# Performance work log

Hardware: AMD Instinct MI355X
Metric: run time of the kernel (lower is better)

The kernel has to match this reference:

```python
import jax, jax.numpy as jnp
import numpy as np

D_MODEL = 1024
HEADS = 16
DEPTH = D_MODEL // HEADS
B, S = 4, 4096
EPS_K = 1e-6  # kernel feature epsilon
EPS_LN = 1e-6


def setup_inputs() -> dict:
    key = jax.random.key(0)
    ks = jax.random.split(key, 8)
    lecun = 1.0 / np.sqrt(D_MODEL)  # LecunNormal stddev
    glorot = np.sqrt(2.0 / (D_MODEL + D_MODEL))  # keras Dense default
    return {
        "q": jax.random.normal(ks[0], (B, S, D_MODEL), jnp.float32),
        "k": jax.random.normal(ks[1], (B, S, D_MODEL), jnp.float32),
        "v": jax.random.normal(ks[2], (B, S, D_MODEL), jnp.float32),
        "mask": jnp.ones((B, S), jnp.float32),
        "wq": jax.random.normal(ks[3], (D_MODEL, D_MODEL), jnp.float32) * lecun,
        "wk": jax.random.normal(ks[4], (D_MODEL, D_MODEL), jnp.float32) * lecun,
        "wv": jax.random.normal(ks[5], (D_MODEL, D_MODEL), jnp.float32) * lecun,
        "ln_gamma": jnp.ones((D_MODEL,), jnp.float32),
        "ln_beta": jnp.zeros((D_MODEL,), jnp.float32),
        "dense_w": jax.random.normal(ks[6], (D_MODEL, D_MODEL), jnp.float32) * glorot,
        "dense_b": jnp.zeros((D_MODEL,), jnp.float32),
    }


def _layernorm(x, g, b):
    m = jnp.mean(x, axis=-1, keepdims=True)
    var = jnp.var(x, axis=-1, keepdims=True)
    return (x - m) * jax.lax.rsqrt(var + EPS_LN) * g + b


def _split_heads(x):
    bsz, sl, _ = x.shape
    return x.reshape(bsz, sl, HEADS, DEPTH).transpose(0, 2, 1, 3)  # [B,H,S,depth]


def reference(q, k, v, mask, wq, wk, wv, ln_gamma, ln_beta, dense_w, dense_b):
    bsz = q.shape[0]
    em = mask[:, None, :, None]  # [B,1,S,1] broadcast over heads/depth
    qh = _split_heads(_layernorm(q @ wq, ln_gamma, ln_beta))
    kh = _split_heads(_layernorm(k @ wk, ln_gamma, ln_beta))
    vh = _split_heads(_layernorm(v @ wv, ln_gamma, ln_beta))
    q_prime = jax.nn.relu(qh) + EPS_K
    k_prime = (jax.nn.relu(kh) + EPS_K) * em
    vh = vh * em
    kv = jnp.einsum('bhnd,bhne->bhde', k_prime, vh)  # [B,H,depth,depth]
    z = 1.0 / (jnp.einsum('bhnd,bhd->bhn', q_prime, k_prime.sum(axis=-2)) + EPS_K)
    att = jnp.einsum('bhnd,bhde,bhn->bhne', q_prime, kv, z)  # [B,H,S,depth]
    # Faithful to original: reshape WITHOUT transposing heads back.
    att = att.reshape(bsz, -1, D_MODEL)  # [B,S,d_model]
    out = att @ dense_w + dense_b
    return _layernorm(out, ln_gamma, ln_beta)
```

## Files before the change

kernel.cpp:

```cpp
#include <hip/hip_runtime.h>
#include <hip/hip_bf16.h>
#include <stdint.h>

#define D_MODEL 1024
#define S_LEN   4096
#define BATCH   4
#define HEADS   16
#define DEPTH   64
#define ROWS    (BATCH*S_LEN)
#define EPS_K_F 1e-6f
#define EPS_LN_F 1e-6f

typedef __attribute__((ext_vector_type(8))) short short8;
typedef __attribute__((ext_vector_type(4))) float f32x4;

__device__ __forceinline__ unsigned short f2bf(float f) {
  union { float f; unsigned u; } x; x.f = f;
  unsigned r = x.u + 0x7FFF + ((x.u >> 16) & 1);
  return (unsigned short)(r >> 16);
}
__device__ __forceinline__ float bf2f(unsigned short b) {
  union { unsigned u; float f; } x; x.u = ((unsigned)b) << 16;
  return x.f;
}
__device__ __forceinline__ void gload16(const void* g, void* l) {
  __builtin_amdgcn_global_load_lds(
      (const __attribute__((address_space(1))) void*)g,
      (__attribute__((address_space(3))) void*)l, 16, 0, 0);
}

__global__ __launch_bounds__(256) void cvt_f32_bf16_k(
    const float* __restrict__ in, unsigned short* __restrict__ out, int n4) {
  int i = blockIdx.x * 256 + threadIdx.x;
  if (i < n4) {
    float4 v = ((const float4*)in)[i];
    ushort4 o;
    o.x = f2bf(v.x); o.y = f2bf(v.y); o.z = f2bf(v.z); o.w = f2bf(v.w);
    ((ushort4*)out)[i] = o;
  }
}

__global__ __launch_bounds__(256) void wtrans_k(
    const float* __restrict__ W, unsigned short* __restrict__ Wt) {
  __shared__ float tile[32][33];
  int n0 = blockIdx.x * 32, k0 = blockIdx.y * 32;
  int tx = threadIdx.x & 31, ty = threadIdx.x >> 5;
  #pragma unroll
  for (int i = 0; i < 32; i += 8)
    tile[ty + i][tx] = W[(size_t)(k0 + ty + i) * D_MODEL + n0 + tx];
  __syncthreads();
  #pragma unroll
  for (int i = 0; i < 32; i += 8)
    Wt[(size_t)(n0 + ty + i) * D_MODEL + k0 + tx] = f2bf(tile[tx][ty + i]);
}


#define GEMM_EPILOGUE(HASBIAS)                                               \
  if (HASBIAS) {                                                             \
    float bv[4];                                                             \
    _Pragma("unroll")                                                        \
    for (int n = 0; n < 4; ++n)                                              \
      bv[n] = bias[(int)n0 + wcn * 64 + n * 16 + l15];                       \
    _Pragma("unroll")                                                        \
    for (int m = 0; m < 8; ++m)                                              \
      _Pragma("unroll")                                                      \
      for (int n = 0; n < 4; ++n)                                            \
        _Pragma("unroll")                                                    \
        for (int j = 0; j < 4; ++j)                                          \
          acc[m][n][j] += bv[n];                                             \
  }                                                                          \
  int seg = (int)(n0 >> 6) + wcn;                                            \
  _Pragma("unroll")                                                          \
  for (int m = 0; m < 8; ++m) {                                              \
    float s[4], s2[4];                                                       \
    _Pragma("unroll")                                                        \
    for (int j = 0; j < 4; ++j) {                                            \
      float a = 0.f, b = 0.f;                                                \
      _Pragma("unroll")                                                      \
      for (int n = 0; n < 4; ++n) { float x = acc[m][n][j]; a += x; b += x*x; } \
      s[j] = a; s2[j] = b;                                                   \
    }                                                                        \
    _Pragma("unroll")                                                        \
    for (int off = 1; off < 16; off <<= 1) {                                 \
      _Pragma("unroll")                                                      \
      for (int j = 0; j < 4; ++j) {                                          \
        s[j]  += __shfl_xor(s[j],  off);                                     \
        s2[j] += __shfl_xor(s2[j], off);                                     \
      }                                                                      \
    }                                                                        \
    if (l15 == 0) {                                                          \
      _Pragma("unroll")                                                      \
      for (int j = 0; j < 4; ++j) {                                          \
        int rg = (int)m0 + wr * 128 + m * 16 + lhi * 4 + j;                  \
        psum[rg * 16 + seg] = s[j];                                          \
        psq [rg * 16 + seg] = s2[j];                                         \
      }                                                                      \
    }                                                                        \
  }                                                                          \
  _Pragma("unroll")                                                          \
  for (int m = 0; m < 8; ++m)                                                \
    _Pragma("unroll")                                                        \
    for (int j = 0; j < 4; ++j) {                                            \
      size_t row = m0 + wr * 128 + m * 16 + lhi * 4 + j;                     \
      _Pragma("unroll")                                                      \
      for (int n = 0; n < 4; ++n) {                                          \
        int col = (int)n0 + wcn * 64 + n * 16 + l15;                         \
        Cb[row * N + col] = f2bf(acc[m][n][j]);                              \
      }                                                                      \
    }

#define STAGE_HALF(kof_, slot_, h_) do {                                     \
    _Pragma("unroll")                                                        \
    for (int j = 0; j < 2; ++j) {                                            \
      int idx = j * 512 + t; int r_ = idx >> 2; int cs_ = idx & 3;           \
      int c_ = cs_ ^ ((r_ >> 1) & 3);                                        \
      gload16(A + (m0 + r_) * (size_t)K + (kof_) + (h_) * 32 + c_ * 8,       \
              &Al[slot_][(h_) * 8192 + idx * 8]);                            \
    }                                                                        \
    _Pragma("unroll")                                                        \
    for (int j = 0; j < 2; ++j) {                                            \
      int idx = j * 512 + t; int r_ = idx >> 2; int cs_ = idx & 3;           \
      int c_ = cs_ ^ ((r_ >> 1) & 3);                                        \
      gload16(Bt + (n0 + r_) * (size_t)K + (kof_) + (h_) * 32 + c_ * 8,      \
              &Bl[slot_][(h_) * 8192 + idx * 8]);                            \
    }                                                                        \
  } while (0)

#define PH_READ_B(kk_)                                                       \
    _Pragma("unroll")                                                        \
    for (int n = 0; n < 4; ++n) {                                            \
      int rb_ = wcn * 64 + n * 16 + l15;                                     \
      bfr[n] = *(const short8*)&Bl[slot][(kk_) * 8192 + rb_ * 32 + cswz];    \
    }
#define PH_READ_A(kk_, mh_)                                                  \
    _Pragma("unroll")                                                        \
    for (int m = 0; m < 4; ++m) {                                            \
      int ra_ = wr * 128 + ((mh_) * 4 + m) * 16 + l15;                       \
      af[m] = *(const short8*)&Al[slot][(kk_) * 8192 + ra_ * 32 + cswz];     \
    }
#define PH_MFMA(mh_)                                                         \
    __builtin_amdgcn_s_setprio(1);                                           \
    _Pragma("unroll")                                                        \
    for (int m = 0; m < 4; ++m)                                              \
      _Pragma("unroll")                                                      \
      for (int n = 0; n < 4; ++n)                                            \
        acc[(mh_) * 4 + m][n] = __builtin_amdgcn_mfma_f32_16x16x32_bf16(     \
            af[m], bfr[n], acc[(mh_) * 4 + m][n], 0, 0, 0);                  \
    __builtin_amdgcn_s_setprio(0);
#define LGKM0                                                                \
    asm volatile("s_waitcnt lgkmcnt(0)" ::: "memory");                       \
    __builtin_amdgcn_sched_barrier(0);

#define SIDE_PACK_STORE(chunk_) do {                                         \
    uint4 pk_;                                                               \
    pk_.x = (unsigned)f2bf(sreg0.x) | ((unsigned)f2bf(sreg0.y) << 16);       \
    pk_.y = (unsigned)f2bf(sreg0.z) | ((unsigned)f2bf(sreg0.w) << 16);       \
    pk_.z = (unsigned)f2bf(sreg1.x) | ((unsigned)f2bf(sreg1.y) << 16);       \
    pk_.w = (unsigned)f2bf(sreg1.z) | ((unsigned)f2bf(sreg1.w) << 16);       \
    *(uint4*)(side_dst + sbase + (size_t)(chunk_) * 4096) = pk_;             \
  } while (0)
#define SIDE_LOAD(chunk_) do {                                               \
    const float* sp_ = side_src + sbase + (size_t)(chunk_) * 4096;           \
    sreg0 = *(const float4*)sp_; sreg1 = *(const float4*)(sp_ + 4);          \
  } while (0)

#define TAIL_TILE(slot_) do {                                                \
    const int slot = (slot_);                                                \
    short8 af[4], bfr[4];                                                    \
    PH_READ_B(0) PH_READ_A(0, 0) LGKM0 PH_MFMA(0)                            \
    PH_READ_A(0, 1) LGKM0 PH_MFMA(1)                                         \
    PH_READ_B(1) PH_READ_A(1, 0) LGKM0 PH_MFMA(0)                            \
    PH_READ_A(1, 1) LGKM0 PH_MFMA(1)                                         \
  } while (0)

template <bool SIDECAR>
__global__ __launch_bounds__(512) void gemm_bt_k(
    const unsigned short* __restrict__ A,
    const unsigned short* __restrict__ Bt,
    unsigned short* __restrict__ Cb,
    float* __restrict__ psum, float* __restrict__ psq,
    const float* __restrict__ bias,
    const float* __restrict__ side_src,
    unsigned short* __restrict__ side_dst,
    int M, int N, int K) {
  __shared__ unsigned short Al[2][16384];
  __shared__ unsigned short Bl[2][16384];
  int t = threadIdx.x;
  int lane = t & 63, wid = t >> 6;
  int wr = wid >> 2, wcn = wid & 3;
  int l15 = lane & 15, lhi = lane >> 4;
  const int cswz = (lhi ^ ((l15 >> 1) & 3)) << 3;
  int p = blockIdx.x;
  int cb = (p >> 3) & 3;
  int rb = (p & 7) | ((p >> 5) << 3);
  size_t m0 = (size_t)rb * 256, n0 = (size_t)cb * 256;
  f32x4 acc[8][4] = {};

  const int KT = K >> 6;

  float4 sreg0 = {}, sreg1 = {};
  size_t sbase = (size_t)p * 65536 + (size_t)t * 8;

  if (SIDECAR) SIDE_LOAD(0);
  STAGE_HALF(0, 0, 0);  STAGE_HALF(0, 0, 1);
  STAGE_HALF(64, 1, 0); STAGE_HALF(64, 1, 1);
  asm volatile("s_waitcnt vmcnt(8)" ::: "memory");
  __builtin_amdgcn_s_barrier();
  __builtin_amdgcn_sched_barrier(0);

  for (int kt = 0; kt < KT - 2; ++kt) {
    const int slot = kt & 1;
    short8 af[4], bfr[4];
    PH_READ_B(0)
    PH_READ_A(0, 0)
    LGKM0
    PH_MFMA(0)
    PH_READ_A(0, 1)
    LGKM0
    __builtin_amdgcn_s_barrier();
    __builtin_amdgcn_sched_barrier(0);
    STAGE_HALF((kt + 2) << 6, slot, 0);
    __builtin_amdgcn_sched_barrier(0);
    PH_MFMA(1)
    PH_READ_B(1)
    PH_READ_A(1, 0)
    LGKM0
    PH_MFMA(0)
    PH_READ_A(1, 1)
    LGKM0
    __builtin_amdgcn_s_barrier();
    __builtin_amdgcn_sched_barrier(0);
    STAGE_HALF((kt + 2) << 6, slot, 1);
    __builtin_amdgcn_sched_barrier(0);
    PH_MFMA(1)
    if (SIDECAR) {
      SIDE_PACK_STORE(kt);
      SIDE_LOAD(kt + 1);
      __builtin_amdgcn_sched_barrier(0);
      asm volatile("s_waitcnt vmcnt(11)" ::: "memory");
    } else {
      asm volatile("s_waitcnt vmcnt(8)" ::: "memory");
    }
    __builtin_amdgcn_s_barrier();
    __builtin_amdgcn_sched_barrier(0);
  }

  TAIL_TILE((KT - 2) & 1);
  if (SIDECAR) {
    SIDE_PACK_STORE(KT - 2);
    SIDE_LOAD(KT - 1);
    __builtin_amdgcn_sched_barrier(0);
    asm volatile("s_waitcnt vmcnt(3)" ::: "memory");
  } else {
    asm volatile("s_waitcnt vmcnt(0)" ::: "memory");
  }
  __builtin_amdgcn_s_barrier();
  __builtin_amdgcn_sched_barrier(0);

  TAIL_TILE((KT - 1) & 1);
  if (SIDECAR) SIDE_PACK_STORE(KT - 1);

  GEMM_EPILOGUE(bias != nullptr)
}

__global__ __launch_bounds__(256) void ln_act_k(
    const unsigned short* __restrict__ Cb,
    const float* __restrict__ psum, const float* __restrict__ psq,
    const float* __restrict__ gamma, const float* __restrict__ beta,
    const float* __restrict__ mask,
    unsigned short* __restrict__ out, int mode) {
  int row = blockIdx.x;
  int t = threadIdx.x;
  float s = 0.f, s2 = 0.f;
  #pragma unroll
  for (int i = 0; i < 16; ++i) { s += psum[row * 16 + i]; s2 += psq[row * 16 + i]; }
  float mean = s * (1.f / D_MODEL);
  float var = s2 * (1.f / D_MODEL) - mean * mean;
  float rstd = rsqrtf(var + EPS_LN_F);
  float mk = (mode > 0) ? mask[row] : 1.f;
  ushort4 cv = ((const ushort4*)(Cb + (size_t)row * D_MODEL))[t];
  float4 gv = ((const float4*)gamma)[t];
  float4 bv = ((const float4*)beta)[t];
  float av[4] = {bf2f(cv.x), bf2f(cv.y), bf2f(cv.z), bf2f(cv.w)};
  float g4[4] = {gv.x, gv.y, gv.z, gv.w};
  float b4[4] = {bv.x, bv.y, bv.z, bv.w};
  unsigned short ov[4];
  #pragma unroll
  for (int j = 0; j < 4; ++j) {
    float ln = (av[j] - mean) * rstd * g4[j] + b4[j];
    if (mode == 0)      ln = fmaxf(ln, 0.f) + EPS_K_F;
    else if (mode == 1) ln = (fmaxf(ln, 0.f) + EPS_K_F) * mk;
    else                ln = ln * mk;
    ov[j] = f2bf(ln);
  }
  ushort4 o; o.x = ov[0]; o.y = ov[1]; o.z = ov[2]; o.w = ov[3];
  ((ushort4*)(out + (size_t)row * D_MODEL))[t] = o;
}

__global__ __launch_bounds__(256) void ln_final_k(
    const unsigned short* __restrict__ Cb,
    const float* __restrict__ psum, const float* __restrict__ psq,
    const float* __restrict__ gamma, const float* __restrict__ beta,
    float* __restrict__ out) {
  int row = blockIdx.x;
  int t = threadIdx.x;
  float s = 0.f, s2 = 0.f;
  #pragma unroll
  for (int i = 0; i < 16; ++i) { s += psum[row * 16 + i]; s2 += psq[row * 16 + i]; }
  float mean = s * (1.f / D_MODEL);
  float var = s2 * (1.f / D_MODEL) - mean * mean;
  float rstd = rsqrtf(var + EPS_LN_F);
  ushort4 cv = ((const ushort4*)(Cb + (size_t)row * D_MODEL))[t];
  float4 gv = ((const float4*)gamma)[t];
  float4 bv = ((const float4*)beta)[t];
  float4 w;
  w.x = (bf2f(cv.x) - mean) * rstd * gv.x + bv.x;
  w.y = (bf2f(cv.y) - mean) * rstd * gv.y + bv.y;
  w.z = (bf2f(cv.z) - mean) * rstd * gv.z + bv.z;
  w.w = (bf2f(cv.w) - mean) * rstd * gv.w + bv.w;
  ((float4*)(out + (size_t)row * D_MODEL))[t] = w;
}

__global__ __launch_bounds__(256) void kv_mfma_k(
    const unsigned short* __restrict__ Kp, const unsigned short* __restrict__ Vp,
    float* __restrict__ part, float* __restrict__ kspart) {
  __shared__ unsigned short Kl[4096];
  __shared__ unsigned short Vl[4096];
  int bh = blockIdx.y, chunk = blockIdx.x;
  int b_ = bh >> 4, h = bh & 15;
  int t = threadIdx.x, lane = t & 63, w = t >> 6;
  int l15 = lane & 15, g = lane >> 4;

  int sn = t >> 2, sd16 = t & 3;
  int sc = sd16 ^ ((sn >> 3) & 3);
  size_t goff = (size_t)sn * D_MODEL + h * DEPTH + sd16 * 16;
  int ldst = sn * 64 + sc * 16;

  short8 ones;
  #pragma unroll
  for (int i = 0; i < 8; ++i) ones[i] = (short)0x3F80;

  f32x4 acc[4] = {};
  f32x4 ks = {};

  int baseA = ((w ^ g) << 4) + l15;
  int baseB0 = ((0 ^ g) << 4) + l15;
  int baseB1 = ((1 ^ g) << 4) + l15;
  int baseB2 = ((2 ^ g) << 4) + l15;
  int baseB3 = ((3 ^ g) << 4) + l15;

  size_t rowbase = ((size_t)b_ * S_LEN + (size_t)chunk * 512) * D_MODEL;
  for (int tile = 0; tile < 8; ++tile) {
    const unsigned short* kg = Kp + rowbase + (size_t)tile * 64 * D_MODEL + goff;
    const unsigned short* vg = Vp + rowbase + (size_t)tile * 64 * D_MODEL + goff;
    uint4 ra = *(const uint4*)kg;
    uint4 rb = *(const uint4*)(kg + 8);
    uint4 rc = *(const uint4*)vg;
    uint4 rd = *(const uint4*)(vg + 8);
    __syncthreads();
    *(uint4*)&Kl[ldst]     = ra;
    *(uint4*)&Kl[ldst + 8] = rb;
    *(uint4*)&Vl[ldst]     = rc;
    *(uint4*)&Vl[ldst + 8] = rd;
    __syncthreads();
    #pragma unroll
    for (int kk = 0; kk < 2; ++kk) {
      int nb = (kk * 32 + g * 8) * 64;
      short8 af, bf0, bf1, bf2, bf3;
      #pragma unroll
      for (int i = 0; i < 8; ++i) {
        int rowoff = nb + i * 64;
        af[i]  = (short)Kl[rowoff + baseA];
        bf0[i] = (short)Vl[rowoff + baseB0];
        bf1[i] = (short)Vl[rowoff + baseB1];
        bf2[i] = (short)Vl[rowoff + baseB2];
        bf3[i] = (short)Vl[rowoff + baseB3];
      }
      acc[0] = __builtin_amdgcn_mfma_f32_16x16x32_bf16(af, bf0, acc[0], 0, 0, 0);
      acc[1] = __builtin_amdgcn_mfma_f32_16x16x32_bf16(af, bf1, acc[1], 0, 0, 0);
      acc[2] = __builtin_amdgcn_mfma_f32_16x16x32_bf16(af, bf2, acc[2], 0, 0, 0);
      acc[3] = __builtin_amdgcn_mfma_f32_16x16x32_bf16(af, bf3, acc[3], 0, 0, 0);
      ks     = __builtin_amdgcn_mfma_f32_16x16x32_bf16(af, ones, ks, 0, 0, 0);
    }
  }
  float* pp = part + ((size_t)bh * 8 + chunk) * 4096;
  #pragma unroll
  for (int nf = 0; nf < 4; ++nf)
    #pragma unroll
    for (int r = 0; r < 4; ++r)
      pp[(16 * w + 4 * g + r) * 64 + 16 * nf + l15] = acc[nf][r];
  if (l15 == 0) {
    #pragma unroll
    for (int r = 0; r < 4; ++r)
      kspart[((size_t)bh * 8 + chunk) * 64 + 16 * w + 4 * g + r] = ks[r];
  }
}

__global__ __launch_bounds__(256) void kv_reduce_k(
    const float* __restrict__ part, const float* __restrict__ kspart,
    unsigned short* __restrict__ KVT, float* __restrict__ ksum) {
  int bh = blockIdx.x, t = threadIdx.x;
  for (int idx = t; idx < 4096; idx += 256) {
    int d = idx >> 6, e = idx & 63;
    float s = 0.f;
    #pragma unroll
    for (int c = 0; c < 8; ++c)
      s += part[((size_t)bh * 8 + c) * 4096 + d * 64 + e];
    KVT[(size_t)bh * 4096 + e * 64 + d] = f2bf(s);
  }
  if (t < 64) {
    float s = 0.f;
    #pragma unroll
    for (int c = 0; c < 8; ++c) s += kspart[((size_t)bh * 8 + c) * 64 + t];
    ksum[bh * 64 + t] = s;
  }
}

__global__ __launch_bounds__(256) void att_k(
    const unsigned short* __restrict__ Qp, const unsigned short* __restrict__ KVT,
    const float* __restrict__ ksum, unsigned short* __restrict__ att) {
  __shared__ unsigned short Ql[128 * 64];
  __shared__ unsigned short Kl[64 * 64];
  __shared__ float ksl[64];
  __shared__ float zl[128];
  int bh = blockIdx.y;
  int b = bh >> 4, h = bh & 15;
  int r0 = blockIdx.x * 128;
  int t = threadIdx.x, lane = t & 63, wid = t >> 6;
  int l15 = lane & 15, lhi = lane >> 4;
  #pragma unroll
  for (int i = 0; i < 4; ++i) {
    int cid = i * 256 + t;
    int r = cid >> 3, c8 = cid & 7;
    gload16(Qp + ((size_t)(b * S_LEN + r0 + r)) * D_MODEL + h * DEPTH + c8 * 8,
            &Ql[cid * 8]);
  }
  #pragma unroll
  for (int i = 0; i < 2; ++i) {
    int cid = i * 256 + t;
    gload16(KVT + (size_t)bh * 4096 + cid * 8, &Kl[cid * 8]);
  }
  if (t < 64) ksl[t] = ksum[bh * 64 + t];
  asm volatile("s_waitcnt vmcnt(0)" ::: "memory");
  __syncthreads();
  {
    int r = t >> 1, half = t & 1;
    float s = 0.f;
    #pragma unroll
    for (int j = 0; j < 32; ++j)
      s += bf2f(Ql[r * 64 + half * 32 + j]) * ksl[half * 32 + j];
    s += __shfl_xor(s, 1);
    if (half == 0) zl[r] = 1.f / (s + EPS_K_F);
  }
  __syncthreads();
  f32x4 acc[2][4] = {};
  #pragma unroll
  for (int kk = 0; kk < 2; ++kk) {
    short8 af[2], bfr[4];
    #pragma unroll
    for (int m = 0; m < 2; ++m)
      af[m] = *(const short8*)&Ql[(wid * 32 + m * 16 + l15) * 64 + kk * 32 + lhi * 8];
    #pragma unroll
    for (int n = 0; n < 4; ++n)
      bfr[n] = *(const short8*)&Kl[(n * 16 + l15) * 64 + kk * 32 + lhi * 8];
    #pragma unroll
    for (int m = 0; m < 2; ++m)
      #pragma unroll
      for (int n = 0; n < 4; ++n)
        acc[m][n] = __builtin_amdgcn_mfma_f32_16x16x32_bf16(af[m], bfr[n], acc[m][n], 0, 0, 0);
  }
  #pragma unroll
  for (int m = 0; m < 2; ++m)
    #pragma unroll
    for (int j = 0; j < 4; ++j) {
      int rl = wid * 32 + m * 16 + lhi * 4 + j;
      int n = r0 + rl;
      float z = zl[rl];
      #pragma unroll
      for (int nf = 0; nf < 4; ++nf) {
        int ee = nf * 16 + l15;
        size_t orow = (size_t)b * S_LEN + h * 256 + (n >> 4);
        int ocol = (n & 15) * 64 + ee;
        att[orow * D_MODEL + ocol] = f2bf(acc[m][nf][j] * z);
      }
    }
}

extern "C" void kernel_launch(void* const* d_in, const int* in_sizes, int n_in,
                              void* d_out, int out_size, void* d_ws, size_t ws_size,
                              hipStream_t stream) {
  (void)in_sizes; (void)n_in; (void)out_size; (void)ws_size;
  const float* q     = (const float*)d_in[0];
  const float* k     = (const float*)d_in[1];
  const float* v     = (const float*)d_in[2];
  const float* mask  = (const float*)d_in[3];
  const float* wq    = (const float*)d_in[4];
  const float* wk    = (const float*)d_in[5];
  const float* wv    = (const float*)d_in[6];
  const float* gamma = (const float*)d_in[7];
  const float* beta  = (const float*)d_in[8];
  const float* dw    = (const float*)d_in[9];
  const float* db    = (const float*)d_in[10];
  float* out = (float*)d_out;

  char* ws = (char*)d_ws;
  unsigned short* Xq  = (unsigned short*)(ws);
  unsigned short* Xk  = (unsigned short*)(ws + 33554432);
  unsigned short* Xv  = (unsigned short*)(ws + 67108864);
  unsigned short* Qp  = Xq;
  unsigned short* Kp  = Xk;
  unsigned short* Vp  = Xv;
  unsigned short* Cd  = Xq;
  unsigned short* WqT = (unsigned short*)(ws + 100663296);
  unsigned short* WkT = WqT + 1048576;
  unsigned short* WvT = WkT + 1048576;
  unsigned short* WdT = WvT + 1048576;
  float* part   = (float*)(ws + 109051904);
  float* kspart = (float*)(ws + 117440512);
  unsigned short* KVT = (unsigned short*)(ws + 117964800);
  float* ksum = (float*)(ws + 118489088);
  float* psum = (float*)(ws + 119537664);
  float* psq  = (float*)(ws + 120586240);
  unsigned short* Cqkv = (unsigned short*)d_out;

  dim3 b256(256);
  dim3 b512(512);
  int n4 = ROWS * D_MODEL / 4;
  dim3 cvtg(n4 / 256);
  dim3 wtg(32, 32);
  dim3 gemmg(256);
  dim3 lng(ROWS);

  wtrans_k<<<wtg, b256, 0, stream>>>(wq, WqT);
  wtrans_k<<<wtg, b256, 0, stream>>>(wk, WkT);
  wtrans_k<<<wtg, b256, 0, stream>>>(wv, WvT);
  wtrans_k<<<wtg, b256, 0, stream>>>(dw, WdT);

  cvt_f32_bf16_k<<<cvtg, b256, 0, stream>>>(q, Xq, n4);

  gemm_bt_k<true><<<gemmg, b512, 0, stream>>>(Xq, WqT, Cqkv, psum, psq, nullptr,
                                              k, Xk, ROWS, D_MODEL, D_MODEL);
  ln_act_k<<<lng, b256, 0, stream>>>(Cqkv, psum, psq, gamma, beta, nullptr, Qp, 0);

  gemm_bt_k<true><<<gemmg, b512, 0, stream>>>(Xk, WkT, Cqkv, psum, psq, nullptr,
                                              v, Xv, ROWS, D_MODEL, D_MODEL);
  ln_act_k<<<lng, b256, 0, stream>>>(Cqkv, psum, psq, gamma, beta, mask, Kp, 1);

  gemm_bt_k<false><<<gemmg, b512, 0, stream>>>(Xv, WvT, Cqkv, psum, psq, nullptr,
                                               nullptr, nullptr, ROWS, D_MODEL, D_MODEL);
  ln_act_k<<<lng, b256, 0, stream>>>(Cqkv, psum, psq, gamma, beta, mask, Vp, 2);

  kv_mfma_k<<<dim3(8, 64), b256, 0, stream>>>(Kp, Vp, part, kspart);
  kv_reduce_k<<<dim3(64), b256, 0, stream>>>(part, kspart, KVT, ksum);
  att_k<<<dim3(32, 64), b256, 0, stream>>>(Qp, KVT, ksum, Cqkv);

  gemm_bt_k<false><<<gemmg, b512, 0, stream>>>(Cqkv, WdT, Cd, psum, psq, db,
                                               nullptr, nullptr, ROWS, D_MODEL, D_MODEL);
  ln_final_k<<<lng, b256, 0, stream>>>(Cd, psum, psq, gamma, beta, out);
}
```

Measured before the change: 347.3 us.

## Fuse layernorm epilogues into GEMMs using a cooperative grid-wide sync

Each projection GEMM and the final dense GEMM now keep their accumulators in registers. They write per-row partial sums, wait on a cooperative-groups grid barrier, then apply layernorm, activation and mask directly before storing. This removes the intermediate bf16 GEMM output and the four separate layernorm kernels, along with their global memory round-trips and launches. In exchange it needs cooperative launches whose whole grid is resident at once, pays for a grid-wide barrier, and holds the accumulators across that barrier.

New measurement: 488.1 us. 40.5% more time.

```diff
diff --git a/kernel.cpp b/kernel.cpp
--- a/kernel.cpp
+++ b/kernel.cpp
@@ -1,5 +1,6 @@
 #include <hip/hip_runtime.h>
 #include <hip/hip_bf16.h>
+#include <hip/hip_cooperative_groups.h>
 #include <stdint.h>
 
 #define D_MODEL 1024
@@ -11,6 +12,8 @@
 #define EPS_K_F 1e-6f
 #define EPS_LN_F 1e-6f
 
+namespace cg = cooperative_groups;
+
 typedef __attribute__((ext_vector_type(8))) short short8;
 typedef __attribute__((ext_vector_type(4))) float f32x4;
 
@@ -55,73 +58,19 @@
 }
 
 
-#define GEMM_EPILOGUE(HASBIAS)                                               \
-  if (HASBIAS) {                                                             \
-    float bv[4];                                                             \
-    _Pragma("unroll")                                                        \
-    for (int n = 0; n < 4; ++n)                                              \
-      bv[n] = bias[(int)n0 + wcn * 64 + n * 16 + l15];                       \
-    _Pragma("unroll")                                                        \
-    for (int m = 0; m < 8; ++m)                                              \
-      _Pragma("unroll")                                                      \
-      for (int n = 0; n < 4; ++n)                                            \
-        _Pragma("unroll")                                                    \
-        for (int j = 0; j < 4; ++j)                                          \
-          acc[m][n][j] += bv[n];                                             \
-  }                                                                          \
-  int seg = (int)(n0 >> 6) + wcn;                                            \
-  _Pragma("unroll")                                                          \
-  for (int m = 0; m < 8; ++m) {                                              \
-    float s[4], s2[4];                                                       \
-    _Pragma("unroll")                                                        \
-    for (int j = 0; j < 4; ++j) {                                            \
-      float a = 0.f, b = 0.f;                                                \
-      _Pragma("unroll")                                                      \
-      for (int n = 0; n < 4; ++n) { float x = acc[m][n][j]; a += x; b += x*x; } \
-      s[j] = a; s2[j] = b;                                                   \
-    }                                                                        \
-    _Pragma("unroll")                                                        \
-    for (int off = 1; off < 16; off <<= 1) {                                 \
-      _Pragma("unroll")                                                      \
-      for (int j = 0; j < 4; ++j) {                                          \
-        s[j]  += __shfl_xor(s[j],  off);                                     \
-        s2[j] += __shfl_xor(s2[j], off);                                     \
-      }                                                                      \
-    }                                                                        \
-    if (l15 == 0) {                                                          \
-      _Pragma("unroll")                                                      \
-      for (int j = 0; j < 4; ++j) {                                          \
-        int rg = (int)m0 + wr * 128 + m * 16 + lhi * 4 + j;                  \
-        psum[rg * 16 + seg] = s[j];                                          \
-        psq [rg * 16 + seg] = s2[j];                                         \
-      }                                                                      \
-    }                                                                        \
-  }                                                                          \
-  _Pragma("unroll")                                                          \
-  for (int m = 0; m < 8; ++m)                                                \
-    _Pragma("unroll")                                                        \
-    for (int j = 0; j < 4; ++j) {                                            \
-      size_t row = m0 + wr * 128 + m * 16 + lhi * 4 + j;                     \
-      _Pragma("unroll")                                                      \
-      for (int n = 0; n < 4; ++n) {                                          \
-        int col = (int)n0 + wcn * 64 + n * 16 + l15;                         \
-        Cb[row * N + col] = f2bf(acc[m][n][j]);                              \
-      }                                                                      \
-    }
-
 #define STAGE_HALF(kof_, slot_, h_) do {                                     \
     _Pragma("unroll")                                                        \
     for (int j = 0; j < 2; ++j) {                                            \
       int idx = j * 512 + t; int r_ = idx >> 2; int cs_ = idx & 3;           \
       int c_ = cs_ ^ ((r_ >> 1) & 3);                                        \
-      gload16(A + (m0 + r_) * (size_t)K + (kof_) + (h_) * 32 + c_ * 8,       \
+      gload16(A + (m0 + r_) * (size_t)D_MODEL + (kof_) + (h_) * 32 + c_ * 8, \
               &Al[slot_][(h_) * 8192 + idx * 8]);                            \
     }                                                                        \
     _Pragma("unroll")                                                        \
     for (int j = 0; j < 2; ++j) {                                            \
       int idx = j * 512 + t; int r_ = idx >> 2; int cs_ = idx & 3;           \
       int c_ = cs_ ^ ((r_ >> 1) & 3);                                        \
-      gload16(Bt + (n0 + r_) * (size_t)K + (kof_) + (h_) * 32 + c_ * 8,      \
+      gload16(Bt + (n0 + r_) * (size_t)D_MODEL + (kof_) + (h_) * 32 + c_ * 8,\
               &Bl[slot_][(h_) * 8192 + idx * 8]);                            \
     }                                                                        \
   } while (0)
@@ -173,16 +122,17 @@
     PH_READ_A(1, 1) LGKM0 PH_MFMA(1)                                         \
   } while (0)
 
-template <bool SIDECAR>
-__global__ __launch_bounds__(512) void gemm_bt_k(
+template <bool SIDECAR, int MODE>
+__global__ __launch_bounds__(512) void gemm_fused_k(
     const unsigned short* __restrict__ A,
     const unsigned short* __restrict__ Bt,
-    unsigned short* __restrict__ Cb,
     float* __restrict__ psum, float* __restrict__ psq,
     const float* __restrict__ bias,
     const float* __restrict__ side_src,
     unsigned short* __restrict__ side_dst,
-    int M, int N, int K) {
+    const float* __restrict__ gamma, const float* __restrict__ beta,
+    const float* __restrict__ maskp,
+    unsigned short* __restrict__ outb, float* __restrict__ outf) {
   __shared__ unsigned short Al[2][16384];
   __shared__ unsigned short Bl[2][16384];
   int t = threadIdx.x;
@@ -196,7 +146,7 @@
   size_t m0 = (size_t)rb * 256, n0 = (size_t)cb * 256;
   f32x4 acc[8][4] = {};
 
-  const int KT = K >> 6;
+  const int KT = D_MODEL >> 6;
 
   float4 sreg0 = {}, sreg1 = {};
   size_t sbase = (size_t)p * 65536 + (size_t)t * 8;
@@ -260,65 +210,94 @@
   TAIL_TILE((KT - 1) & 1);
   if (SIDECAR) SIDE_PACK_STORE(KT - 1);
 
-  GEMM_EPILOGUE(bias != nullptr)
-}
-
-__global__ __launch_bounds__(256) void ln_act_k(
-    const unsigned short* __restrict__ Cb,
-    const float* __restrict__ psum, const float* __restrict__ psq,
-    const float* __restrict__ gamma, const float* __restrict__ beta,
-    const float* __restrict__ mask,
-    unsigned short* __restrict__ out, int mode) {
-  int row = blockIdx.x;
-  int t = threadIdx.x;
-  float s = 0.f, s2 = 0.f;
-  #pragma unroll
-  for (int i = 0; i < 16; ++i) { s += psum[row * 16 + i]; s2 += psq[row * 16 + i]; }
-  float mean = s * (1.f / D_MODEL);
-  float var = s2 * (1.f / D_MODEL) - mean * mean;
-  float rstd = rsqrtf(var + EPS_LN_F);
-  float mk = (mode > 0) ? mask[row] : 1.f;
-  ushort4 cv = ((const ushort4*)(Cb + (size_t)row * D_MODEL))[t];
-  float4 gv = ((const float4*)gamma)[t];
-  float4 bv = ((const float4*)beta)[t];
-  float av[4] = {bf2f(cv.x), bf2f(cv.y), bf2f(cv.z), bf2f(cv.w)};
-  float g4[4] = {gv.x, gv.y, gv.z, gv.w};
-  float b4[4] = {bv.x, bv.y, bv.z, bv.w};
-  unsigned short ov[4];
-  #pragma unroll
-  for (int j = 0; j < 4; ++j) {
-    float ln = (av[j] - mean) * rstd * g4[j] + b4[j];
-    if (mode == 0)      ln = fmaxf(ln, 0.f) + EPS_K_F;
-    else if (mode == 1) ln = (fmaxf(ln, 0.f) + EPS_K_F) * mk;
-    else                ln = ln * mk;
-    ov[j] = f2bf(ln);
-  }
-  ushort4 o; o.x = ov[0]; o.y = ov[1]; o.z = ov[2]; o.w = ov[3];
-  ((ushort4*)(out + (size_t)row * D_MODEL))[t] = o;
-}
-
-__global__ __launch_bounds__(256) void ln_final_k(
-    const unsigned short* __restrict__ Cb,
-    const float* __restrict__ psum, const float* __restrict__ psq,
-    const float* __restrict__ gamma, const float* __restrict__ beta,
-    float* __restrict__ out) {
-  int row = blockIdx.x;
-  int t = threadIdx.x;
-  float s = 0.f, s2 = 0.f;
-  #pragma unroll
-  for (int i = 0; i < 16; ++i) { s += psum[row * 16 + i]; s2 += psq[row * 16 + i]; }
-  float mean = s * (1.f / D_MODEL);
-  float var = s2 * (1.f / D_MODEL) - mean * mean;
-  float rstd = rsqrtf(var + EPS_LN_F);
-  ushort4 cv = ((const ushort4*)(Cb + (size_t)row * D_MODEL))[t];
-  float4 gv = ((const float4*)gamma)[t];
-  float4 bv = ((const float4*)beta)[t];
-  float4 w;
-  w.x = (bf2f(cv.x) - mean) * rstd * gv.x + bv.x;
-  w.y = (bf2f(cv.y) - mean) * rstd * gv.y + bv.y;
-  w.z = (bf2f(cv.z) - mean) * rstd * gv.z + bv.z;
-  w.w = (bf2f(cv.w) - mean) * rstd * gv.w + bv.w;
-  ((float4*)(out + (size_t)row * D_MODEL))[t] = w;
+  if (MODE == 3) {
+    float bv[4];
+    #pragma unroll
+    for (int n = 0; n < 4; ++n)
+      bv[n] = bias[(int)n0 + wcn * 64 + n * 16 + l15];
+    #pragma unroll
+    for (int m = 0; m < 8; ++m)
+      #pragma unroll
+      for (int n = 0; n < 4; ++n)
+        #pragma unroll
+        for (int j = 0; j < 4; ++j)
+          acc[m][n][j] += bv[n];
+  }
+
+  {
+    int seg = (int)(n0 >> 6) + wcn;
+    #pragma unroll
+    for (int m = 0; m < 8; ++m) {
+      float s[4], s2[4];
+      #pragma unroll
+      for (int j = 0; j < 4; ++j) {
+        float a = 0.f, b = 0.f;
+        #pragma unroll
+        for (int n = 0; n < 4; ++n) { float x = acc[m][n][j]; a += x; b += x * x; }
+        s[j] = a; s2[j] = b;
+      }
+      #pragma unroll
+      for (int off = 1; off < 16; off <<= 1) {
+        #pragma unroll
+        for (int j = 0; j < 4; ++j) {
+          s[j]  += __shfl_xor(s[j],  off);
+          s2[j] += __shfl_xor(s2[j], off);
+        }
+      }
+      if (l15 == 0) {
+        #pragma unroll
+        for (int j = 0; j < 4; ++j) {
+          int rg = (int)m0 + wr * 128 + m * 16 + lhi * 4 + j;
+          psum[rg * 16 + seg] = s[j];
+          psq [rg * 16 + seg] = s2[j];
+        }
+      }
+    }
+  }
+
+  cg::this_grid().sync();
+
+  float* meanl = (float*)&Al[0][0];
+  float* rstdl = meanl + 256;
+  float* maskl = rstdl + 256;
+  for (int r = t; r < 256; r += 512) {
+    int row = (int)m0 + r;
+    float s = 0.f, s2 = 0.f;
+    #pragma unroll
+    for (int i = 0; i < 16; ++i) { s += psum[row * 16 + i]; s2 += psq[row * 16 + i]; }
+    float mean = s * (1.f / D_MODEL);
+    float var = s2 * (1.f / D_MODEL) - mean * mean;
+    meanl[r] = mean;
+    rstdl[r] = rsqrtf(var + EPS_LN_F);
+    if (MODE == 1 || MODE == 2) maskl[r] = maskp[row];
+  }
+  __syncthreads();
+
+  float gv[4], bv2[4];
+  #pragma unroll
+  for (int n = 0; n < 4; ++n) {
+    int col = (int)n0 + wcn * 64 + n * 16 + l15;
+    gv[n] = gamma[col]; bv2[n] = beta[col];
+  }
+  #pragma unroll
+  for (int m = 0; m < 8; ++m)
+    #pragma unroll
+    for (int j = 0; j < 4; ++j) {
+      int rl = wr * 128 + m * 16 + lhi * 4 + j;
+      size_t row = m0 + rl;
+      float mean = meanl[rl], rstd = rstdl[rl];
+      float mk = (MODE == 1 || MODE == 2) ? maskl[rl] : 1.f;
+      #pragma unroll
+      for (int n = 0; n < 4; ++n) {
+        int col = (int)n0 + wcn * 64 + n * 16 + l15;
+        float ln = (acc[m][n][j] - mean) * rstd * gv[n] + bv2[n];
+        if (MODE == 0)      ln = fmaxf(ln, 0.f) + EPS_K_F;
+        else if (MODE == 1) ln = (fmaxf(ln, 0.f) + EPS_K_F) * mk;
+        else if (MODE == 2) ln = ln * mk;
+        if (MODE == 3) outf[row * D_MODEL + col] = ln;
+        else           outb[row * D_MODEL + col] = f2bf(ln);
+      }
+    }
 }
 
 __global__ __launch_bounds__(256) void kv_mfma_k(
@@ -510,7 +489,6 @@
   unsigned short* Qp  = Xq;
   unsigned short* Kp  = Xk;
   unsigned short* Vp  = Xv;
-  unsigned short* Cd  = Xq;
   unsigned short* WqT = (unsigned short*)(ws + 100663296);
   unsigned short* WkT = WqT + 1048576;
   unsigned short* WvT = WkT + 1048576;
@@ -523,14 +501,19 @@
   float* psq  = (float*)(ws + 120586240);
   unsigned short* Cqkv = (unsigned short*)d_out;
 
+  const float* nob = nullptr;
+  const float* nosrc = nullptr;
+  unsigned short* nodst = nullptr;
+  unsigned short* noub = nullptr;
+  float* nouf = nullptr;
+
   dim3 b256(256);
   dim3 b512(512);
   int n4 = ROWS * D_MODEL / 4;
   dim3 cvtg(n4 / 256);
   dim3 wtg(32, 32);
   dim3 gemmg(256);
-  dim3 lng(ROWS);
-
+  
   wtrans_k<<<wtg, b256, 0, stream>>>(wq, WqT);
   wtrans_k<<<wtg, b256, 0, stream>>>(wk, WkT);
   wtrans_k<<<wtg, b256, 0, stream>>>(wv, WvT);
@@ -538,23 +521,33 @@
 
   cvt_f32_bf16_k<<<cvtg, b256, 0, stream>>>(q, Xq, n4);
 
-  gemm_bt_k<true><<<gemmg, b512, 0, stream>>>(Xq, WqT, Cqkv, psum, psq, nullptr,
-                                              k, Xk, ROWS, D_MODEL, D_MODEL);
-  ln_act_k<<<lng, b256, 0, stream>>>(Cqkv, psum, psq, gamma, beta, nullptr, Qp, 0);
-
-  gemm_bt_k<true><<<gemmg, b512, 0, stream>>>(Xk, WkT, Cqkv, psum, psq, nullptr,
-                                              v, Xv, ROWS, D_MODEL, D_MODEL);
-  ln_act_k<<<lng, b256, 0, stream>>>(Cqkv, psum, psq, gamma, beta, mask, Kp, 1);
-
-  gemm_bt_k<false><<<gemmg, b512, 0, stream>>>(Xv, WvT, Cqkv, psum, psq, nullptr,
-                                               nullptr, nullptr, ROWS, D_MODEL, D_MODEL);
-  ln_act_k<<<lng, b256, 0, stream>>>(Cqkv, psum, psq, gamma, beta, mask, Vp, 2);
+  {
+    void* a[] = {(void*)&Xq, (void*)&WqT, (void*)&psum, (void*)&psq, (void*)&nob,
+                 (void*)&k, (void*)&Xk, (void*)&gamma, (void*)&beta, (void*)&mask,
+                 (void*)&Qp, (void*)&nouf};
+    hipLaunchCooperativeKernel((void*)gemm_fused_k<true, 0>, gemmg, b512, a, 0, stream);
+  }
+  {
+    void* a[] = {(void*)&Xk, (void*)&WkT, (void*)&psum, (void*)&psq, (void*)&nob,
+                 (void*)&v, (void*)&Xv, (void*)&gamma, (void*)&beta, (void*)&mask,
+                 (void*)&Kp, (void*)&nouf};
+    hipLaunchCooperativeKernel((void*)gemm_fused_k<true, 1>, gemmg, b512, a, 0, stream);
+  }
+  {
+    void* a[] = {(void*)&Xv, (void*)&WvT, (void*)&psum, (void*)&psq, (void*)&nob,
+                 (void*)&nosrc, (void*)&nodst, (void*)&gamma, (void*)&beta, (void*)&mask,
+                 (void*)&Vp, (void*)&nouf};
+    hipLaunchCooperativeKernel((void*)gemm_fused_k<false, 2>, gemmg, b512, a, 0, stream);
+  }
 
   kv_mfma_k<<<dim3(8, 64), b256, 0, stream>>>(Kp, Vp, part, kspart);
   kv_reduce_k<<<dim3(64), b256, 0, stream>>>(part, kspart, KVT, ksum);
   att_k<<<dim3(32, 64), b256, 0, stream>>>(Qp, KVT, ksum, Cqkv);
 
-  gemm_bt_k<false><<<gemmg, b512, 0, stream>>>(Cqkv, WdT, Cd, psum, psq, db,
-                                               nullptr, nullptr, ROWS, D_MODEL, D_MODEL);
-  ln_final_k<<<lng, b256, 0, stream>>>(Cd, psum, psq, gamma, beta, out);
-}
+  {
+    void* a[] = {(void*)&Cqkv, (void*)&WdT, (void*)&psum, (void*)&psq, (void*)&db,
+                 (void*)&nosrc, (void*)&nodst, (void*)&gamma, (void*)&beta, (void*)&mask,
+                 (void*)&noub, (void*)&out};
+    hipLaunchCooperativeKernel((void*)gemm_fused_k<false, 3>, gemmg, b512, a, 0, stream);
+  }
+}
```
